# Kernel optimization log

Measured on AMD Instinct MI355X. Metric: run time of the kernel, lower is better.

## Reference

```python
import jax, jax.numpy as jnp
import numpy as np

N = 50000        # nodes
E = 800000       # edges (avg degree 16)
H = 64           # hidden_dim


def setup_inputs() -> dict:
    key = jax.random.key(0)
    k1, k2, k3, k4 = jax.random.split(key, 4)
    node_emb = jax.random.normal(k1, (N, H), dtype=jnp.float32)
    edge_index = jax.random.randint(k2, (2, E), 0, N, dtype=jnp.int64)
    # MLP params: Linear(2H -> H), ReLU, Linear(H -> 1)
    W1 = jax.random.normal(k3, (2 * H, H), dtype=jnp.float32) / np.sqrt(2 * H)
    b1 = jnp.zeros((H,), dtype=jnp.float32)
    W2 = jax.random.normal(k4, (H, 1), dtype=jnp.float32) / np.sqrt(H)
    b2 = jnp.zeros((1,), dtype=jnp.float32)
    return {"node_emb": node_emb, "edge_index": edge_index,
            "W1": W1, "b1": b1, "W2": W2, "b2": b2}


def reference(node_emb, edge_index, W1, b1, W2, b2):
    # Gather endpoint embeddings: [E, H] each
    src = node_emb[edge_index[0]]
    dst = node_emb[edge_index[1]]
    edge_feat = jnp.concatenate([src, dst], axis=-1)      # [E, 2H]
    h = jax.nn.relu(edge_feat @ W1 + b1)                   # [E, H]
    logits = (h @ W2 + b2).squeeze(-1)                     # [E]
    return logits
```

## Files before the change

kernel.cpp:

```cpp
#include <hip/hip_runtime.h>
#include <hip/hip_bf16.h>


typedef __attribute__((ext_vector_type(8))) short bf16x8;
typedef __attribute__((ext_vector_type(4))) float f32x4;

__device__ __forceinline__ unsigned short f2bf(float f) {
    union { float f; unsigned int i; } v;
    v.f = f;
    unsigned int r = v.i + 0x7fffu + ((v.i >> 16) & 1u);
    return (unsigned short)(r >> 16);
}

template <int N>
__device__ __forceinline__ float dpp_shr(float x) {
    return __int_as_float(__builtin_amdgcn_update_dpp(
        0, __float_as_int(x), 0x110 | N, 0xf, 0xf, true));
}

__global__ __launch_bounds__(256) void precompute_ab(
    const float* __restrict__ emb, const float* __restrict__ W1,
    const float* __restrict__ b1, unsigned short* __restrict__ AB,
    int nNodes, int totalWaves)
{
    const int lane = threadIdx.x & 63;
    const int waveId = blockIdx.x * (blockDim.x >> 6) + (threadIdx.x >> 6);
    const int c  = lane & 15;
    const int kb = lane >> 4;

    bf16x8 wfrag[8][2];
    float bias[8];
#pragma unroll
    for (int nt = 0; nt < 8; ++nt) {
        const int jp = nt * 16 + c;
        const float* wcol = (jp < 64) ? (W1 + jp) : (W1 + 64 * 64 + (jp - 64));
        bias[nt] = (jp < 64) ? b1[jp] : 0.f;
#pragma unroll
        for (int kk = 0; kk < 2; ++kk) {
#pragma unroll
            for (int i = 0; i < 8; ++i) {
                const int k = kk * 32 + kb * 8 + i;
                wfrag[nt][kk][i] = (short)f2bf(wcol[(size_t)k * 64]);
            }
        }
    }

    for (int n0 = waveId * 16; n0 < nNodes; n0 += totalWaves * 16) {
        const int arow = n0 + c;
        const int arow_c = (arow < nNodes) ? arow : (nNodes - 1);
        const float* erow = emb + (size_t)arow_c * 64 + kb * 8;
        bf16x8 afrag[2];
#pragma unroll
        for (int kk = 0; kk < 2; ++kk) {
            const float4 f0 = *reinterpret_cast<const float4*>(erow + kk * 32);
            const float4 f1 = *reinterpret_cast<const float4*>(erow + kk * 32 + 4);
            afrag[kk][0] = (short)f2bf(f0.x); afrag[kk][1] = (short)f2bf(f0.y);
            afrag[kk][2] = (short)f2bf(f0.z); afrag[kk][3] = (short)f2bf(f0.w);
            afrag[kk][4] = (short)f2bf(f1.x); afrag[kk][5] = (short)f2bf(f1.y);
            afrag[kk][6] = (short)f2bf(f1.z); afrag[kk][7] = (short)f2bf(f1.w);
        }

        f32x4 acc[8];
#pragma unroll
        for (int nt = 0; nt < 8; ++nt) {
            acc[nt][0] = bias[nt]; acc[nt][1] = bias[nt];
            acc[nt][2] = bias[nt]; acc[nt][3] = bias[nt];
        }
#pragma unroll
        for (int kk = 0; kk < 2; ++kk)
#pragma unroll
            for (int nt = 0; nt < 8; ++nt)
                acc[nt] = __builtin_amdgcn_mfma_f32_16x16x32_bf16(
                    afrag[kk], wfrag[nt][kk], acc[nt], 0, 0, 0);

        if (n0 + 16 <= nNodes) {
#pragma unroll
            for (int nt = 0; nt < 8; ++nt) {
                const int jp = nt * 16 + c;
#pragma unroll
                for (int r = 0; r < 4; ++r) {
                    const int node = n0 + kb * 4 + r;
                    AB[(size_t)node * 128 + jp] = f2bf(acc[nt][r]);
                }
            }
        } else {
#pragma unroll
            for (int nt = 0; nt < 8; ++nt) {
                const int jp = nt * 16 + c;
#pragma unroll
                for (int r = 0; r < 4; ++r) {
                    const int node = n0 + kb * 4 + r;
                    if (node < nNodes) AB[(size_t)node * 128 + jp] = f2bf(acc[nt][r]);
                }
            }
        }
    }
}

__global__ __launch_bounds__(256) void edge_mlp(
    const int* __restrict__ ei, const unsigned int* __restrict__ AB,
    const float* __restrict__ W2, const float* __restrict__ b2,
    float* __restrict__ out, int nEdges, int totalWaves)
{
    const int lane = threadIdx.x & 63;
    const int sub  = lane & 7;
    const int grp  = lane >> 3;
    const int waveId = blockIdx.x * (blockDim.x >> 6) + (threadIdx.x >> 6);

    float w2v[8];
#pragma unroll
    for (int j = 0; j < 8; ++j) w2v[j] = W2[sub * 8 + j];
    const float b2s = b2[0];
    const int stride = totalWaves * 8;

#pragma unroll 8
    for (int base = waveId * 8; base < nEdges; base += stride) {
        const int e = base + grp;
        const bool valid = (e < nEdges);
        const int ec = valid ? e : 0;

        const int src = ei[ec];
        const int dst = ei[nEdges + ec];

        const uint4 ua = *reinterpret_cast<const uint4*>(AB + (size_t)src * 64 + sub * 4);
        const uint4 ub = *reinterpret_cast<const uint4*>(AB + (size_t)dst * 64 + 32 + sub * 4);

        float p = 0.f;
        const unsigned int au[4] = {ua.x, ua.y, ua.z, ua.w};
        const unsigned int bu[4] = {ub.x, ub.y, ub.z, ub.w};
#pragma unroll
        for (int i = 0; i < 4; ++i) {
            const float alo = __int_as_float((int)(au[i] << 16));
            const float ahi = __int_as_float((int)(au[i] & 0xffff0000u));
            const float blo = __int_as_float((int)(bu[i] << 16));
            const float bhi = __int_as_float((int)(bu[i] & 0xffff0000u));
            const float h0 = fmaxf(alo + blo, 0.f);
            const float h1 = fmaxf(ahi + bhi, 0.f);
            p = fmaf(h0, w2v[2 * i], p);
            p = fmaf(h1, w2v[2 * i + 1], p);
        }

        p += dpp_shr<1>(p);
        p += dpp_shr<2>(p);
        p += dpp_shr<4>(p);

        if (valid && sub == 7) out[e] = p + b2s;
    }
}

extern "C" void kernel_launch(void* const* d_in, const int* in_sizes, int n_in,
                              void* d_out, int out_size, void* d_ws, size_t ws_size,
                              hipStream_t stream) {
    const float* emb = (const float*)d_in[0];
    const int*   ei  = (const int*)d_in[1];
    const float* W1  = (const float*)d_in[2];
    const float* b1  = (const float*)d_in[3];
    const float* W2  = (const float*)d_in[4];
    const float* b2  = (const float*)d_in[5];
    float* out = (float*)d_out;
    unsigned short* AB = (unsigned short*)d_ws;

    const int nNodes = in_sizes[0] / 64;
    const int nEdges = in_sizes[1] / 2;

    {
        const int blocks = 256;
        precompute_ab<<<blocks, 256, 0, stream>>>(emb, W1, b1, AB, nNodes, blocks * 4);
    }
    {
        const int blocks = 2048;
        edge_mlp<<<blocks, 256, 0, stream>>>(ei, (const unsigned int*)AB, W2, b2,
                                             out, nEdges, blocks * 4);
    }
}
```

Baseline: 102.7 us.

## Stage W1 via LDS, coalesce AB stores, and software-pipeline edge index loads

New measurement: 108.7 us. 5.9% more time.

```diff
diff --git a/kernel.cpp b/kernel.cpp
--- a/kernel.cpp
+++ b/kernel.cpp
@@ -23,32 +23,45 @@
     const float* __restrict__ b1, unsigned short* __restrict__ AB,
     int nNodes, int totalWaves)
 {
-    const int lane = threadIdx.x & 63;
-    const int waveId = blockIdx.x * (blockDim.x >> 6) + (threadIdx.x >> 6);
+    __shared__ unsigned short WT[128][72];
+    __shared__ unsigned short stage[4][16][136];
+
+    const int tid  = threadIdx.x;
+    const int lane = tid & 63;
+    const int wv   = tid >> 6;
+    const int waveId = blockIdx.x * 4 + wv;
     const int c  = lane & 15;
     const int kb = lane >> 4;
 
+    for (int p = tid; p < 2048; p += 256) {
+        const float4 v = reinterpret_cast<const float4*>(W1)[p];
+        const int k  = p >> 4;
+        const int j0 = (p & 15) * 4;
+        const int kk2 = (k < 64) ? k : (k - 64);
+        const int jo  = (k < 64) ? 0 : 64;
+        WT[jo + j0 + 0][kk2] = f2bf(v.x);
+        WT[jo + j0 + 1][kk2] = f2bf(v.y);
+        WT[jo + j0 + 2][kk2] = f2bf(v.z);
+        WT[jo + j0 + 3][kk2] = f2bf(v.w);
+    }
+    __syncthreads();
+
     bf16x8 wfrag[8][2];
     float bias[8];
 #pragma unroll
     for (int nt = 0; nt < 8; ++nt) {
         const int jp = nt * 16 + c;
-        const float* wcol = (jp < 64) ? (W1 + jp) : (W1 + 64 * 64 + (jp - 64));
         bias[nt] = (jp < 64) ? b1[jp] : 0.f;
 #pragma unroll
-        for (int kk = 0; kk < 2; ++kk) {
-#pragma unroll
-            for (int i = 0; i < 8; ++i) {
-                const int k = kk * 32 + kb * 8 + i;
-                wfrag[nt][kk][i] = (short)f2bf(wcol[(size_t)k * 64]);
-            }
-        }
-    }
-
-    for (int n0 = waveId * 16; n0 < nNodes; n0 += totalWaves * 16) {
+        for (int kk = 0; kk < 2; ++kk)
+            wfrag[nt][kk] = *reinterpret_cast<const bf16x8*>(&WT[jp][kk * 32 + kb * 8]);
+    }
+
+    const int nTiles = (nNodes + 15) >> 4;
+    for (int t = waveId; t < nTiles; t += totalWaves) {
+        const int n0 = t * 16;
         const int arow = n0 + c;
-        const int arow_c = (arow < nNodes) ? arow : (nNodes - 1);
-        const float* erow = emb + (size_t)arow_c * 64 + kb * 8;
+        const float* erow = emb + (size_t)((arow < nNodes) ? arow : (nNodes - 1)) * 64 + kb * 8;
         bf16x8 afrag[2];
 #pragma unroll
         for (int kk = 0; kk < 2; ++kk) {
@@ -73,28 +86,49 @@
                 acc[nt] = __builtin_amdgcn_mfma_f32_16x16x32_bf16(
                     afrag[kk], wfrag[nt][kk], acc[nt], 0, 0, 0);
 
+#pragma unroll
+        for (int nt = 0; nt < 8; ++nt) {
+            const int col = nt * 16 + c;
+#pragma unroll
+            for (int r = 0; r < 4; ++r)
+                stage[wv][kb * 4 + r][col] = f2bf(acc[nt][r]);
+        }
+        uint4* dst4 = reinterpret_cast<uint4*>(AB + (size_t)n0 * 128);
         if (n0 + 16 <= nNodes) {
 #pragma unroll
-            for (int nt = 0; nt < 8; ++nt) {
-                const int jp = nt * 16 + c;
-#pragma unroll
-                for (int r = 0; r < 4; ++r) {
-                    const int node = n0 + kb * 4 + r;
-                    AB[(size_t)node * 128 + jp] = f2bf(acc[nt][r]);
-                }
+            for (int s2 = 0; s2 < 4; ++s2) {
+                const int q = s2 * 64 + lane;
+                dst4[q] = *reinterpret_cast<const uint4*>(&stage[wv][q >> 4][(q & 15) * 8]);
             }
         } else {
 #pragma unroll
-            for (int nt = 0; nt < 8; ++nt) {
-                const int jp = nt * 16 + c;
-#pragma unroll
-                for (int r = 0; r < 4; ++r) {
-                    const int node = n0 + kb * 4 + r;
-                    if (node < nNodes) AB[(size_t)node * 128 + jp] = f2bf(acc[nt][r]);
-                }
+            for (int s2 = 0; s2 < 4; ++s2) {
+                const int q = s2 * 64 + lane;
+                if (n0 + (q >> 4) < nNodes)
+                    dst4[q] = *reinterpret_cast<const uint4*>(&stage[wv][q >> 4][(q & 15) * 8]);
             }
         }
     }
+}
+
+__device__ __forceinline__ float edge_dot(const uint4 ua, const uint4 ub,
+                                          const float* __restrict__ w2v) {
+    float p = 0.f;
+    const unsigned int au[4] = {ua.x, ua.y, ua.z, ua.w};
+    const unsigned int bu[4] = {ub.x, ub.y, ub.z, ub.w};
+#pragma unroll
+    for (int i = 0; i < 4; ++i) {
+        const float alo = __int_as_float((int)(au[i] << 16));
+        const float ahi = __int_as_float((int)(au[i] & 0xffff0000u));
+        const float blo = __int_as_float((int)(bu[i] << 16));
+        const float bhi = __int_as_float((int)(bu[i] & 0xffff0000u));
+        p = fmaf(fmaxf(alo + blo, 0.f), w2v[2 * i], p);
+        p = fmaf(fmaxf(ahi + bhi, 0.f), w2v[2 * i + 1], p);
+    }
+    p += dpp_shr<1>(p);
+    p += dpp_shr<2>(p);
+    p += dpp_shr<4>(p);
+    return p;
 }
 
 __global__ __launch_bounds__(256) void edge_mlp(
@@ -111,40 +145,47 @@
 #pragma unroll
     for (int j = 0; j < 8; ++j) w2v[j] = W2[sub * 8 + j];
     const float b2s = b2[0];
-    const int stride = totalWaves * 8;
-
-#pragma unroll 8
-    for (int base = waveId * 8; base < nEdges; base += stride) {
-        const int e = base + grp;
-        const bool valid = (e < nEdges);
-        const int ec = valid ? e : 0;
-
-        const int src = ei[ec];
-        const int dst = ei[nEdges + ec];
-
-        const uint4 ua = *reinterpret_cast<const uint4*>(AB + (size_t)src * 64 + sub * 4);
-        const uint4 ub = *reinterpret_cast<const uint4*>(AB + (size_t)dst * 64 + 32 + sub * 4);
-
-        float p = 0.f;
-        const unsigned int au[4] = {ua.x, ua.y, ua.z, ua.w};
-        const unsigned int bu[4] = {ub.x, ub.y, ub.z, ub.w};
-#pragma unroll
-        for (int i = 0; i < 4; ++i) {
-            const float alo = __int_as_float((int)(au[i] << 16));
-            const float ahi = __int_as_float((int)(au[i] & 0xffff0000u));
-            const float blo = __int_as_float((int)(bu[i] << 16));
-            const float bhi = __int_as_float((int)(bu[i] & 0xffff0000u));
-            const float h0 = fmaxf(alo + blo, 0.f);
-            const float h1 = fmaxf(ahi + bhi, 0.f);
-            p = fmaf(h0, w2v[2 * i], p);
-            p = fmaf(h1, w2v[2 * i + 1], p);
-        }
-
-        p += dpp_shr<1>(p);
-        p += dpp_shr<2>(p);
-        p += dpp_shr<4>(p);
-
-        if (valid && sub == 7) out[e] = p + b2s;
+    const int stride = totalWaves * 16;
+
+    int base = waveId * 16;
+    if (base >= nEdges) return;
+
+    int eA = base + grp, eB = base + 8 + grp;
+    int ecA = (eA < nEdges) ? eA : 0;
+    int ecB = (eB < nEdges) ? eB : 0;
+    int srcA = __builtin_nontemporal_load(ei + ecA);
+    int dstA = __builtin_nontemporal_load(ei + nEdges + ecA);
+    int srcB = __builtin_nontemporal_load(ei + ecB);
+    int dstB = __builtin_nontemporal_load(ei + nEdges + ecB);
+
+    while (true) {
+        const uint4 uaA = *reinterpret_cast<const uint4*>(AB + (size_t)srcA * 64 + sub * 4);
+        const uint4 ubA = *reinterpret_cast<const uint4*>(AB + (size_t)dstA * 64 + 32 + sub * 4);
+        const uint4 uaB = *reinterpret_cast<const uint4*>(AB + (size_t)srcB * 64 + sub * 4);
+        const uint4 ubB = *reinterpret_cast<const uint4*>(AB + (size_t)dstB * 64 + 32 + sub * 4);
+
+        const int curA = base + grp, curB = base + 8 + grp;
+        const int nbase = base + stride;
+
+        if (nbase < nEdges) {
+            eA = nbase + grp;  eB = nbase + 8 + grp;
+            ecA = (eA < nEdges) ? eA : 0;
+            ecB = (eB < nEdges) ? eB : 0;
+            srcA = __builtin_nontemporal_load(ei + ecA);
+            dstA = __builtin_nontemporal_load(ei + nEdges + ecA);
+            srcB = __builtin_nontemporal_load(ei + ecB);
+            dstB = __builtin_nontemporal_load(ei + nEdges + ecB);
+        }
+
+        const float pA = edge_dot(uaA, ubA, w2v);
+        const float pB = edge_dot(uaB, ubB, w2v);
+        if (sub == 7) {
+            if (curA < nEdges) __builtin_nontemporal_store(pA + b2s, out + curA);
+            if (curB < nEdges) __builtin_nontemporal_store(pB + b2s, out + curB);
+        }
+
+        if (nbase >= nEdges) break;
+        base = nbase;
     }
 }
 
@@ -164,7 +205,7 @@
     const int nEdges = in_sizes[1] / 2;
 
     {
-        const int blocks = 256;
+        const int blocks = 128;
         precompute_ab<<<blocks, 256, 0, stream>>>(emb, W1, b1, AB, nNodes, blocks * 4);
     }
     {
```

## Bucket edges by endpoint low bits so edge MLP gathers hit cache better

Applied to the files above, without the earlier changes.

Measured after the change: 148.4 us. +44.5%, slower.

```diff
diff --git a/kernel.cpp b/kernel.cpp
--- a/kernel.cpp
+++ b/kernel.cpp
@@ -4,6 +4,11 @@
 
 typedef __attribute__((ext_vector_type(8))) short bf16x8;
 typedef __attribute__((ext_vector_type(4))) float f32x4;
+
+#define PRE_BLOCKS  256
+#define HIST_BLOCKS 1024
+#define SCAT_BLOCKS 1024
+#define MLP_BLOCKS  2048
 
 __device__ __forceinline__ unsigned short f2bf(float f) {
     union { float f; unsigned int i; } v;
@@ -18,13 +23,49 @@
         0, __float_as_int(x), 0x110 | N, 0xf, 0xf, true));
 }
 
-__global__ __launch_bounds__(256) void precompute_ab(
+__device__ __forceinline__ float edge_dot(const uint4 ua, const uint4 ub,
+                                          const float* __restrict__ w2v) {
+    float p = 0.f;
+    const unsigned int au[4] = {ua.x, ua.y, ua.z, ua.w};
+    const unsigned int bu[4] = {ub.x, ub.y, ub.z, ub.w};
+#pragma unroll
+    for (int i = 0; i < 4; ++i) {
+        const float alo = __int_as_float((int)(au[i] << 16));
+        const float ahi = __int_as_float((int)(au[i] & 0xffff0000u));
+        const float blo = __int_as_float((int)(bu[i] << 16));
+        const float bhi = __int_as_float((int)(bu[i] & 0xffff0000u));
+        p = fmaf(fmaxf(alo + blo, 0.f), w2v[2 * i], p);
+        p = fmaf(fmaxf(ahi + bhi, 0.f), w2v[2 * i + 1], p);
+    }
+    p += dpp_shr<1>(p);
+    p += dpp_shr<2>(p);
+    p += dpp_shr<4>(p);
+    return p;
+}
+
+__global__ __launch_bounds__(256) void pre_and_hist(
     const float* __restrict__ emb, const float* __restrict__ W1,
     const float* __restrict__ b1, unsigned short* __restrict__ AB,
-    int nNodes, int totalWaves)
+    int nNodes, const int* __restrict__ ei, int nEdges,
+    unsigned int* __restrict__ hist)
 {
+    __shared__ unsigned int h[64];
+    if (blockIdx.x >= PRE_BLOCKS) {
+        const int b = blockIdx.x - PRE_BLOCKS;
+        if (threadIdx.x < 64) h[threadIdx.x] = 0;
+        __syncthreads();
+        for (int e = b * 256 + threadIdx.x; e < nEdges; e += HIST_BLOCKS * 256) {
+            const int s = ei[e], d = ei[nEdges + e];
+            atomicAdd(&h[((s & 7) << 3) | (d & 7)], 1u);
+        }
+        __syncthreads();
+        if (threadIdx.x < 64) atomicAdd(&hist[threadIdx.x], h[threadIdx.x]);
+        return;
+    }
+
     const int lane = threadIdx.x & 63;
-    const int waveId = blockIdx.x * (blockDim.x >> 6) + (threadIdx.x >> 6);
+    const int waveId = blockIdx.x * 4 + (threadIdx.x >> 6);
+    const int totalWaves = PRE_BLOCKS * 4;
     const int c  = lane & 15;
     const int kb = lane >> 4;
 
@@ -36,19 +77,17 @@
         const float* wcol = (jp < 64) ? (W1 + jp) : (W1 + 64 * 64 + (jp - 64));
         bias[nt] = (jp < 64) ? b1[jp] : 0.f;
 #pragma unroll
-        for (int kk = 0; kk < 2; ++kk) {
+        for (int kk = 0; kk < 2; ++kk)
 #pragma unroll
             for (int i = 0; i < 8; ++i) {
                 const int k = kk * 32 + kb * 8 + i;
                 wfrag[nt][kk][i] = (short)f2bf(wcol[(size_t)k * 64]);
             }
-        }
     }
 
     for (int n0 = waveId * 16; n0 < nNodes; n0 += totalWaves * 16) {
         const int arow = n0 + c;
-        const int arow_c = (arow < nNodes) ? arow : (nNodes - 1);
-        const float* erow = emb + (size_t)arow_c * 64 + kb * 8;
+        const float* erow = emb + (size_t)((arow < nNodes) ? arow : (nNodes - 1)) * 64 + kb * 8;
         bf16x8 afrag[2];
 #pragma unroll
         for (int kk = 0; kk < 2; ++kk) {
@@ -78,10 +117,8 @@
             for (int nt = 0; nt < 8; ++nt) {
                 const int jp = nt * 16 + c;
 #pragma unroll
-                for (int r = 0; r < 4; ++r) {
-                    const int node = n0 + kb * 4 + r;
-                    AB[(size_t)node * 128 + jp] = f2bf(acc[nt][r]);
-                }
+                for (int r = 0; r < 4; ++r)
+                    AB[(size_t)(n0 + kb * 4 + r) * 128 + jp] = f2bf(acc[nt][r]);
             }
         } else {
 #pragma unroll
@@ -97,54 +134,90 @@
     }
 }
 
-__global__ __launch_bounds__(256) void edge_mlp(
-    const int* __restrict__ ei, const unsigned int* __restrict__ AB,
+__global__ __launch_bounds__(256) void edge_scatter(
+    const int* __restrict__ ei, int nEdges,
+    const unsigned int* __restrict__ hist, unsigned int* __restrict__ gpos,
+    int4* __restrict__ recs)
+{
+    __shared__ unsigned int lh[64], loff[64], lcnt[64], lbase[64], lrun[64];
+    const int t = threadIdx.x;
+    const int per = (nEdges + SCAT_BLOCKS - 1) / SCAT_BLOCKS;
+    const int e0 = blockIdx.x * per;
+    const int e1 = min(nEdges, e0 + per);
+
+    if (t < 64) { lh[t] = hist[t]; lcnt[t] = 0; lrun[t] = 0; }
+    __syncthreads();
+    if (t < 64) {
+        unsigned int o = 0;
+        for (int k = 0; k < t; ++k) o += lh[k];
+        loff[t] = o;
+    }
+    for (int e = e0 + t; e < e1; e += 256) {
+        const int s = ei[e], d = ei[nEdges + e];
+        atomicAdd(&lcnt[((s & 7) << 3) | (d & 7)], 1u);
+    }
+    __syncthreads();
+    if (t < 64) {
+        const unsigned int c = lcnt[t];
+        lbase[t] = loff[t] + (c ? atomicAdd(&gpos[t], c) : 0u);
+    }
+    __syncthreads();
+    for (int e = e0 + t; e < e1; e += 256) {
+        const int s = ei[e], d = ei[nEdges + e];
+        const int cl = ((s & 7) << 3) | (d & 7);
+        const unsigned int p = lbase[cl] + atomicAdd(&lrun[cl], 1u);
+        recs[p] = make_int4(s, d, e, 0);
+    }
+}
+
+__global__ __launch_bounds__(256) void edge_mlp_sorted(
+    const int4* __restrict__ recs, const unsigned int* __restrict__ AB,
+    const unsigned int* __restrict__ hist,
     const float* __restrict__ W2, const float* __restrict__ b2,
-    float* __restrict__ out, int nEdges, int totalWaves)
+    float* __restrict__ out, int nEdges)
 {
-    const int lane = threadIdx.x & 63;
+    __shared__ unsigned int lh[64], loff[64];
+    const int t = threadIdx.x;
+    if (t < 64) lh[t] = hist[t];
+    __syncthreads();
+    if (t < 64) {
+        unsigned int o = 0;
+        for (int k = 0; k < t; ++k) o += lh[k];
+        loff[t] = o;
+    }
+    __syncthreads();
+
+    const int lane = t & 63;
     const int sub  = lane & 7;
     const int grp  = lane >> 3;
-    const int waveId = blockIdx.x * (blockDim.x >> 6) + (threadIdx.x >> 6);
+    const int wv   = t >> 6;
+    const int i    = blockIdx.x & 7;
+    const int r    = blockIdx.x >> 3;
 
     float w2v[8];
 #pragma unroll
     for (int j = 0; j < 8; ++j) w2v[j] = W2[sub * 8 + j];
     const float b2s = b2[0];
-    const int stride = totalWaves * 8;
-
-#pragma unroll 8
-    for (int base = waveId * 8; base < nEdges; base += stride) {
-        const int e = base + grp;
-        const bool valid = (e < nEdges);
-        const int ec = valid ? e : 0;
-
-        const int src = ei[ec];
-        const int dst = ei[nEdges + ec];
-
-        const uint4 ua = *reinterpret_cast<const uint4*>(AB + (size_t)src * 64 + sub * 4);
-        const uint4 ub = *reinterpret_cast<const uint4*>(AB + (size_t)dst * 64 + 32 + sub * 4);
-
-        float p = 0.f;
-        const unsigned int au[4] = {ua.x, ua.y, ua.z, ua.w};
-        const unsigned int bu[4] = {ub.x, ub.y, ub.z, ub.w};
-#pragma unroll
-        for (int i = 0; i < 4; ++i) {
-            const float alo = __int_as_float((int)(au[i] << 16));
-            const float ahi = __int_as_float((int)(au[i] & 0xffff0000u));
-            const float blo = __int_as_float((int)(bu[i] << 16));
-            const float bhi = __int_as_float((int)(bu[i] & 0xffff0000u));
-            const float h0 = fmaxf(alo + blo, 0.f);
-            const float h1 = fmaxf(ahi + bhi, 0.f);
-            p = fmaf(h0, w2v[2 * i], p);
-            p = fmaf(h1, w2v[2 * i + 1], p);
-        }
-
-        p += dpp_shr<1>(p);
-        p += dpp_shr<2>(p);
-        p += dpp_shr<4>(p);
-
-        if (valid && sub == 7) out[e] = p + b2s;
+
+    for (int j = 0; j < 8; ++j) {
+        const int c = (i << 3) | j;
+        const unsigned int off = loff[c], sz = lh[c];
+        const unsigned int chunk = (sz + 255) >> 8;
+        const unsigned int s0 = off + r * chunk;
+        const unsigned int s1 = min(off + sz, s0 + chunk);
+        const unsigned int wc = (chunk + 3) >> 2;
+        const unsigned int t0 = s0 + wv * wc;
+        const unsigned int t1 = min(s1, t0 + wc);
+
+        for (unsigned int e = t0 + grp; e < t1; e += 8) {
+            const int4 rec = recs[e];
+            const uint4 ua = *reinterpret_cast<const uint4*>(
+                AB + (size_t)rec.x * 64 + sub * 4);
+            const uint4 ub = *reinterpret_cast<const uint4*>(
+                AB + (size_t)rec.y * 64 + 32 + sub * 4);
+            const float p = edge_dot(ua, ub, w2v);
+            if (sub == 7) out[rec.z] = p + b2s;
+        }
     }
 }
 
@@ -158,18 +231,23 @@
     const float* W2  = (const float*)d_in[4];
     const float* b2  = (const float*)d_in[5];
     float* out = (float*)d_out;
-    unsigned short* AB = (unsigned short*)d_ws;
 
     const int nNodes = in_sizes[0] / 64;
     const int nEdges = in_sizes[1] / 2;
 
-    {
-        const int blocks = 256;
-        precompute_ab<<<blocks, 256, 0, stream>>>(emb, W1, b1, AB, nNodes, blocks * 4);
-    }
-    {
-        const int blocks = 2048;
-        edge_mlp<<<blocks, 256, 0, stream>>>(ei, (const unsigned int*)AB, W2, b2,
-                                             out, nEdges, blocks * 4);
-    }
-}
+    char* ws = (char*)d_ws;
+    unsigned short* AB   = (unsigned short*)ws;
+    int4*           recs = (int4*)(ws + (16u << 20));
+    unsigned int*   hist = (unsigned int*)(ws + (32u << 20));
+    unsigned int*   gpos = hist + 64;
+
+    hipMemsetAsync(hist, 0, 2 * 64 * sizeof(unsigned int), stream);
+
+    pre_and_hist<<<PRE_BLOCKS + HIST_BLOCKS, 256, 0, stream>>>(
+        emb, W1, b1, AB, nNodes, ei, nEdges, hist);
+
+    edge_scatter<<<SCAT_BLOCKS, 256, 0, stream>>>(ei, nEdges, hist, gpos, recs);
+
+    edge_mlp_sorted<<<MLP_BLOCKS, 256, 0, stream>>>(
+        recs, (const unsigned int*)AB, hist, W2, b2, out, nEdges);
+}
```
